# Optimization experiments

Measured on AMD Instinct MI355X. Metric: run time of the kernel, lower is better.

The kernel has to match this reference:

```python
import jax, jax.numpy as jnp
import numpy as np

D = 1024
H = 16
HD = D // H
S = 2048
B = 2
INNER = 4 * D
EPS = 1e-5


def _layernorm(x, w, b):
    mu = jnp.mean(x, axis=-1, keepdims=True)
    var = jnp.mean(jnp.square(x - mu), axis=-1, keepdims=True)
    return (x - mu) * jax.lax.rsqrt(var + EPS) * w + b


def _rope(x, cos, sin):
    # x: [B, S, H, HD]; cos/sin: [S, HD//2]
    xe, xo = x[..., 0::2], x[..., 1::2]
    c = cos[None, :, None, :]
    s = sin[None, :, None, :]
    oe = xe * c - xo * s
    oo = xe * s + xo * c
    return jnp.stack([oe, oo], axis=-1).reshape(x.shape)


def setup_inputs() -> dict:
    key = jax.random.key(0)
    ks = jax.random.split(key, 12)
    hidden_states = jax.random.normal(ks[0], (B, S, D), dtype=jnp.float32)
    time_step_emb = jax.random.normal(ks[1], (B, 6 * D), dtype=jnp.float32)
    # causal additive mask [1,1,S,S]
    causal = jnp.tril(jnp.ones((S, S), dtype=bool))
    attention_mask = jnp.where(causal, 0.0, -1e9).astype(jnp.float32)[None, None]
    # proper RoPE tables
    inv_freq = 1.0 / (10000.0 ** (np.arange(0, HD, 2, dtype=np.float32) / HD))
    t = np.arange(S, dtype=np.float32)
    freqs = np.outer(t, inv_freq)  # [S, HD//2]
    rope_cos = jnp.asarray(np.cos(freqs))
    rope_sin = jnp.asarray(np.sin(freqs))
    p = 0.02
    params = dict(
        ln1_w=jnp.ones((D,), jnp.float32), ln1_b=jnp.zeros((D,), jnp.float32),
        ln2_w=jnp.ones((D,), jnp.float32), ln2_b=jnp.zeros((D,), jnp.float32),
        c_attn_w=jax.random.normal(ks[2], (D, 3 * D), jnp.float32) * p,
        c_attn_b=jnp.zeros((3 * D,), jnp.float32),
        c_proj_w=jax.random.normal(ks[3], (D, D), jnp.float32) * p,
        c_proj_b=jnp.zeros((D,), jnp.float32),
        fc_w=jax.random.normal(ks[4], (D, INNER), jnp.float32) * p,
        fc_b=jnp.zeros((INNER,), jnp.float32),
        proj_w=jax.random.normal(ks[5], (INNER, D), jnp.float32) * p,
        proj_b=jnp.zeros((D,), jnp.float32),
        scale_shift_table=jax.random.normal(ks[6], (6, D), jnp.float32) / np.sqrt(D),
    )
    return dict(hidden_states=hidden_states, attention_mask=attention_mask,
                time_step_emb=time_step_emb, rope_cos=rope_cos, rope_sin=rope_sin,
                **params)


def reference(hidden_states, attention_mask, time_step_emb, rope_cos, rope_sin,
              ln1_w, ln1_b, ln2_w, ln2_b, c_attn_w, c_attn_b, c_proj_w, c_proj_b,
              fc_w, fc_b, proj_w, proj_b, scale_shift_table):
    b = hidden_states.shape[0]
    mods = scale_shift_table[None] + time_step_emb.reshape(b, 6, D)  # [B,6,D]
    sh_msa, sc_msa, g_msa, sh_mlp, sc_mlp, g_mlp = [mods[:, i:i + 1] for i in range(6)]

    residual = hidden_states
    h = _layernorm(hidden_states, ln1_w, ln1_b) * (1.0 + sc_msa) + sh_msa

    qkv = h @ c_attn_w + c_attn_b  # [B,S,3D]
    q, k, v = jnp.split(qkv, 3, axis=-1)
    q = _rope(q.reshape(b, S, H, HD), rope_cos, rope_sin)
    k = _rope(k.reshape(b, S, H, HD), rope_cos, rope_sin)
    v = v.reshape(b, S, H, HD)
    scores = jnp.einsum('bqhd,bkhd->bhqk', q, k) / np.sqrt(float(HD))
    scores = scores + attention_mask
    attn = jax.nn.softmax(scores, axis=-1)
    out = jnp.einsum('bhqk,bkhd->bqhd', attn, v).reshape(b, S, D)
    attn_out = out @ c_proj_w + c_proj_b

    hidden = attn_out * g_msa + residual
    residual = hidden
    h = _layernorm(hidden, ln2_w, ln2_b) * (1.0 + sc_mlp) + sh_mlp
    h = jax.nn.gelu(h @ fc_w + fc_b, approximate=True)  # gelu_new (tanh approx)
    h = h @ proj_w + proj_b
    return h * g_mlp + residual
```

## Files before the change

### kernel.cpp

```cpp
#include <hip/hip_runtime.h>
#include <hip/hip_bf16.h>
#include <type_traits>

#define D_MODEL 1024
#define N_HEADS 16
#define HEAD_DIM 64
#define SEQ 2048
#define BATCH 2
#define INNER_DIM 4096
#define ROWS (BATCH*SEQ)

using f32x4  = __attribute__((ext_vector_type(4))) float;
using bf16x8 = __attribute__((ext_vector_type(8))) short;

__device__ __forceinline__ void gl_lds16(const void* g, void* l) {
  __builtin_amdgcn_global_load_lds(
      (const __attribute__((address_space(1))) void*)g,
      (__attribute__((address_space(3))) void*)l, 16, 0, 0);
}

__device__ __forceinline__ float bf2f(unsigned short u) {
  union { unsigned int i; float f; } v; v.i = ((unsigned int)u) << 16; return v.f;
}
__device__ __forceinline__ unsigned short f2bf(float f) {
  union { float f; unsigned int i; } v; v.f = f;
  unsigned int x = v.i;
  return (unsigned short)((x + 0x7fffu + ((x >> 16) & 1u)) >> 16);
}

__device__ __forceinline__ float exp2fast(float x) {
  return __builtin_amdgcn_exp2f(x);
}

__device__ __forceinline__ float gelu_tanh(float x) {
  float x3 = x * x * x;
  float z = 0.7978845608028654f * (x + 0.044715f * x3);
  z = fminf(z, 15.0f);
  float e = __expf(2.0f * z);
  float th = (e - 1.0f) / (e + 1.0f);
  return 0.5f * x * (1.0f + th);
}

__global__ void transpose_convert(const float* __restrict__ in,
                                  unsigned short* __restrict__ out,
                                  int K, int N) {
  __shared__ float tile[32][33];
  int n0 = blockIdx.x * 32, k0 = blockIdx.y * 32;
  int tx = threadIdx.x, ty = threadIdx.y;
#pragma unroll
  for (int i = 0; i < 4; i++)
    tile[ty + i * 8][tx] = in[(size_t)(k0 + ty + i * 8) * N + n0 + tx];
  __syncthreads();
#pragma unroll
  for (int i = 0; i < 4; i++)
    out[(size_t)(n0 + ty + i * 8) * K + k0 + tx] = f2bf(tile[tx][ty + i * 8]);
}

template<int SH_IDX, int SC_IDX>
__global__ void ln_mod_kernel(const float* __restrict__ x,
                              const float* __restrict__ lw,
                              const float* __restrict__ lb,
                              const float* __restrict__ sst,
                              const float* __restrict__ temb,
                              unsigned short* __restrict__ out) {
  int row = blockIdx.x;
  int b = row >> 11;
  int t = threadIdx.x;
  const float* xr = x + (size_t)row * D_MODEL;
  float4 v = ((const float4*)xr)[t];
  float s = v.x + v.y + v.z + v.w;
  float s2 = v.x * v.x + v.y * v.y + v.z * v.z + v.w * v.w;
#pragma unroll
  for (int o = 1; o < 64; o <<= 1) { s += __shfl_xor(s, o); s2 += __shfl_xor(s2, o); }
  __shared__ float red[8];
  int wid = t >> 6, lane = t & 63;
  if (lane == 0) { red[wid] = s; red[4 + wid] = s2; }
  __syncthreads();
  s = red[0] + red[1] + red[2] + red[3];
  s2 = red[4] + red[5] + red[6] + red[7];
  float mu = s * (1.0f / D_MODEL);
  float var = s2 * (1.0f / D_MODEL) - mu * mu;
  float rs = rsqrtf(var + 1e-5f);
  int d0 = t * 4;
  float xv[4] = { v.x, v.y, v.z, v.w };
  ushort4 ov;
  unsigned short* po = (unsigned short*)&ov;
#pragma unroll
  for (int j = 0; j < 4; j++) {
    int d = d0 + j;
    float ln = (xv[j] - mu) * rs * lw[d] + lb[d];
    float sc = sst[SC_IDX * D_MODEL + d] + temb[b * 6 * D_MODEL + SC_IDX * D_MODEL + d];
    float sh = sst[SH_IDX * D_MODEL + d] + temb[b * 6 * D_MODEL + SH_IDX * D_MODEL + d];
    po[j] = f2bf(ln * (1.0f + sc) + sh);
  }
  *((ushort4*)(out + (size_t)row * D_MODEL + d0)) = ov;
}

enum { EPI_QKV = 0, EPI_GELU = 2, EPI_PART = 3 };

template<int EPI, int NK>
__global__ __launch_bounds__(512, 2)
void gemm8p(const unsigned short* __restrict__ A,
            const unsigned short* __restrict__ Bt,
            const float* __restrict__ bias,
            void* __restrict__ Cout,
            int N, int Kstride,
            const float* __restrict__ cosb,
            const float* __restrict__ sinb) {
  extern __shared__ char smem[];
  const int t = threadIdx.x;
  const int w = t >> 6, l = t & 63;
  const int lg = l >> 4, ll = l & 15;
  const int wm = w >> 2, wn = w & 3;

  const int nx = gridDim.x;
  const int nwg = nx * gridDim.y;
  const int lid = blockIdx.y * nx + blockIdx.x;
  const int nid = (lid & 7) * (nwg >> 3) + (lid >> 3);
  const int m0 = (nid / nx) * 256, n0 = (nid % nx) * 256;

  f32x4 acc[8][4] = {};

  const unsigned short* gA[2][2];
  const unsigned short* gB[2][2];
#pragma unroll
  for (int j = 0; j < 2; j++) {
    int c = j * 512 + t, row = c >> 2, ch = c & 3;
    int ks = (ch ^ ((row >> 1) & 3)) << 3;
#pragma unroll
    for (int kh = 0; kh < 2; kh++) {
      gA[kh][j] = A  + (size_t)(m0 + row) * Kstride + kh * 32 + ks;
      gB[kh][j] = Bt + (size_t)(n0 + row) * Kstride + kh * 32 + ks;
    }
  }
  unsigned aoff[8], boff[4];
#pragma unroll
  for (int mf = 0; mf < 8; mf++) {
    int row = wm * 128 + mf * 16 + ll;
    aoff[mf] = row * 64 + ((lg ^ ((row >> 1) & 3)) << 4);
  }
#pragma unroll
  for (int nf = 0; nf < 4; nf++) {
    int row = wn * 64 + nf * 16 + ll;
    boff[nf] = 65536 + row * 64 + ((lg ^ ((row >> 1) & 3)) << 4);
  }

  auto stgA = [&](int kh, int P) {
#pragma unroll
    for (int j = 0; j < 2; j++) {
      gl_lds16(gA[kh][j], smem + P * 32768 + kh * 16384 + (j * 512 + t) * 16);
      gA[kh][j] += 64;
    }
  };
  auto stgB = [&](int kh, int P) {
#pragma unroll
    for (int j = 0; j < 2; j++) {
      gl_lds16(gB[kh][j], smem + 65536 + P * 32768 + kh * 16384 + (j * 512 + t) * 16);
      gB[kh][j] += 64;
    }
  };
  auto mm = [&](int mfb, bf16x8 (&af)[4], bf16x8 (&bk)[4]) {
#pragma unroll
    for (int i = 0; i < 4; i++)
#pragma unroll
      for (int nf = 0; nf < 4; nf++)
        acc[mfb + i][nf] =
            __builtin_amdgcn_mfma_f32_16x16x32_bf16(af[i], bk[nf], acc[mfb + i][nf], 0, 0, 0);
  };

#define GBAR()  asm volatile("" ::: "memory"); __builtin_amdgcn_s_barrier(); \
                asm volatile("" ::: "memory");
#define LGKM0() asm volatile("s_waitcnt lgkmcnt(0)" ::: "memory"); \
                __builtin_amdgcn_sched_barrier(0);

  auto tile = [&](auto PC, bool stg, bool last) {
    constexpr int P = decltype(PC)::value;
    const char* ab = smem + P * 32768;
    bf16x8 af[4], bk[4];
    if (stg) stgA(0, P ^ 1);
    GBAR();
#pragma unroll
    for (int i = 0; i < 4; i++) af[i] = *(const bf16x8*)(ab + aoff[i]);
#pragma unroll
    for (int i = 0; i < 4; i++) bk[i] = *(const bf16x8*)(ab + boff[i]);
    LGKM0();
    __builtin_amdgcn_s_setprio(1); mm(0, af, bk); __builtin_amdgcn_s_setprio(0);
    GBAR();
    if (stg) stgB(0, P ^ 1);
    if (!last) asm volatile("s_waitcnt vmcnt(4)" ::: "memory");
    else       asm volatile("s_waitcnt vmcnt(0)" ::: "memory");
    GBAR();
#pragma unroll
    for (int i = 0; i < 4; i++) af[i] = *(const bf16x8*)(ab + aoff[4 + i]);
    LGKM0();
    __builtin_amdgcn_s_setprio(1); mm(4, af, bk); __builtin_amdgcn_s_setprio(0);
    GBAR();
    if (stg) stgA(1, P ^ 1);
    GBAR();
#pragma unroll
    for (int i = 0; i < 4; i++) af[i] = *(const bf16x8*)(ab + 16384 + aoff[i]);
#pragma unroll
    for (int i = 0; i < 4; i++) bk[i] = *(const bf16x8*)(ab + 16384 + boff[i]);
    LGKM0();
    __builtin_amdgcn_s_setprio(1); mm(0, af, bk); __builtin_amdgcn_s_setprio(0);
    GBAR();
    if (stg) {
      stgB(1, P ^ 1);
      asm volatile("s_waitcnt vmcnt(4)" ::: "memory");
    }
    GBAR();
#pragma unroll
    for (int i = 0; i < 4; i++) af[i] = *(const bf16x8*)(ab + 16384 + aoff[4 + i]);
    LGKM0();
    __builtin_amdgcn_s_setprio(1); mm(4, af, bk); __builtin_amdgcn_s_setprio(0);
    GBAR();
  };

  stgA(0, 0); stgB(0, 0); stgA(1, 0); stgB(1, 0);
  asm volatile("s_waitcnt vmcnt(4)" ::: "memory");
  GBAR();

#pragma unroll 1
  for (int u = 0; u + 2 < NK; u += 2) {
    tile(std::integral_constant<int, 0>{}, true, false);
    tile(std::integral_constant<int, 1>{}, true, false);
  }
  tile(std::integral_constant<int, 0>{}, true, false);
  tile(std::integral_constant<int, 1>{}, false, true);

#pragma unroll
  for (int mf = 0; mf < 8; mf++) {
#pragma unroll
    for (int nf = 0; nf < 4; nf++) {
      int col = n0 + wn * 64 + nf * 16 + ll;
      float bv = (EPI == EPI_PART) ? 0.0f : bias[col];
#pragma unroll
      for (int r = 0; r < 4; r++) {
        int row = m0 + wm * 128 + mf * 16 + lg * 4 + r;
        float v = acc[mf][nf][r] + bv;
        if constexpr (EPI == EPI_QKV) {
          if (col < 2048) {
            float vp = __shfl_xor(v, 1);
            int sp = row & (SEQ - 1);
            int ip = (col & 63) >> 1;
            float cz = cosb[sp * 32 + ip], sz = sinb[sp * 32 + ip];
            float ov = (col & 1) ? (vp * sz + v * cz) : (v * cz - vp * sz);
            if (col < 1024) ov *= 0.18033688011112042f;
            v = ov;
          }
          ((unsigned short*)Cout)[(size_t)row * N + col] = f2bf(v);
        } else if constexpr (EPI == EPI_GELU) {
          ((unsigned short*)Cout)[(size_t)row * N + col] = f2bf(gelu_tanh(v));
        } else {
          ((unsigned short*)Cout)[(size_t)row * N + col] = f2bf(v);
        }
      }
    }
  }
}
#undef GBAR
#undef LGKM0

template<int EPI, int NK>
__global__ __launch_bounds__(256, 2)
void gemm64(const unsigned short* __restrict__ A,
            const unsigned short* __restrict__ Bt,
            const float* __restrict__ bias,
            void* C0, void* C1,
            int N, int Kstride,
            const float* __restrict__ cosb,
            const float* __restrict__ sinb) {
  __shared__ unsigned short Alds[2][128 * 64];
  __shared__ unsigned short Blds[2][128 * 64];
  const int t = threadIdx.x;
  const int w = t >> 6, l = t & 63;
  const int lg = l >> 4, ll = l & 15;
  const int wm = w >> 1, wn = w & 1;
  const int kbase = blockIdx.z * (NK * 64);

  const int nx = gridDim.x;
  const int nwg = nx * gridDim.y;
  const int lid = blockIdx.y * nx + blockIdx.x;
  const int nid = (lid & 7) * (nwg >> 3) + (lid >> 3);
  const int m0 = (nid / nx) * 128, n0 = (nid % nx) * 128;

  void* Cout = blockIdx.z ? C1 : C0;

  f32x4 acc[4][4] = {};

  const unsigned short* ga[4];
  const unsigned short* gb[4];
#pragma unroll
  for (int i = 0; i < 4; i++) {
    int c = i * 256 + t, row = c >> 3, q = c & 7;
    ga[i] = A + (size_t)(m0 + row) * Kstride + kbase + ((q ^ (row & 7)) << 3);
    gb[i] = Bt + (size_t)(n0 + row) * Kstride + kbase + ((q ^ (row & 7)) << 3);
  }
  const unsigned short* ra[4][2];
  const unsigned short* rb[4][2];
#pragma unroll
  for (int f = 0; f < 4; f++) {
    int rowA = wm * 64 + f * 16 + ll;
    int rowB = wn * 64 + f * 16 + ll;
#pragma unroll
    for (int kk = 0; kk < 2; kk++) {
      ra[f][kk] = &Alds[0][rowA * 64 + ((((kk * 4 + lg) ^ (rowA & 7))) << 3)];
      rb[f][kk] = &Blds[0][rowB * 64 + ((((kk * 4 + lg) ^ (rowB & 7))) << 3)];
    }
  }

#pragma unroll
  for (int i = 0; i < 4; i++) {
    gl_lds16(ga[i], (char*)&Alds[0][0] + (i * 256 + t) * 16); ga[i] += 64;
  }
#pragma unroll
  for (int i = 0; i < 4; i++) {
    gl_lds16(gb[i], (char*)&Blds[0][0] + (i * 256 + t) * 16); gb[i] += 64;
  }

  auto giter = [&](auto BUFC, bool last) {
    constexpr int BUF = decltype(BUFC)::value;
    constexpr int NBUF = BUF ^ 1;
    if (!last) {
#pragma unroll
      for (int i = 0; i < 4; i++) {
        gl_lds16(ga[i], (char*)&Alds[NBUF][0] + (i * 256 + t) * 16); ga[i] += 64;
      }
#pragma unroll
      for (int i = 0; i < 4; i++) {
        gl_lds16(gb[i], (char*)&Blds[NBUF][0] + (i * 256 + t) * 16); gb[i] += 64;
      }
      asm volatile("s_waitcnt vmcnt(8)" ::: "memory");
    } else {
      asm volatile("s_waitcnt vmcnt(0)" ::: "memory");
    }
    __builtin_amdgcn_s_barrier();
    asm volatile("" ::: "memory");
#pragma unroll
    for (int kk = 0; kk < 2; kk++) {
      bf16x8 af[4], bfr[4];
#pragma unroll
      for (int mf = 0; mf < 4; mf++)
        af[mf] = *(const bf16x8*)(ra[mf][kk] + BUF * 8192);
#pragma unroll
      for (int nf = 0; nf < 4; nf++)
        bfr[nf] = *(const bf16x8*)(rb[nf][kk] + BUF * 8192);
#pragma unroll
      for (int mf = 0; mf < 4; mf++)
#pragma unroll
        for (int nf = 0; nf < 4; nf++)
          acc[mf][nf] = __builtin_amdgcn_mfma_f32_16x16x32_bf16(af[mf], bfr[nf], acc[mf][nf], 0, 0, 0);
    }
    asm volatile("" ::: "memory");
    __builtin_amdgcn_s_barrier();
  };

#pragma unroll 1
  for (int u = 0; u < NK - 2; u += 2) {
    giter(std::integral_constant<int, 0>{}, false);
    giter(std::integral_constant<int, 1>{}, false);
  }
  giter(std::integral_constant<int, 0>{}, false);
  giter(std::integral_constant<int, 1>{}, true);

#pragma unroll
  for (int mf = 0; mf < 4; mf++) {
#pragma unroll
    for (int nf = 0; nf < 4; nf++) {
      int col = n0 + wn * 64 + nf * 16 + ll;
#pragma unroll
      for (int r = 0; r < 4; r++) {
        int row = m0 + wm * 64 + mf * 16 + lg * 4 + r;
        float v = acc[mf][nf][r];
        ((unsigned short*)Cout)[(size_t)row * N + col] = f2bf(v);
      }
    }
  }
}

__global__ void reduce_ln(const unsigned short* __restrict__ p0,
                          const unsigned short* __restrict__ p1,
                          const float* __restrict__ bias,
                          const float* __restrict__ sst,
                          const float* __restrict__ temb,
                          const float* __restrict__ resid,
                          float* __restrict__ hidden,
                          const float* __restrict__ lw,
                          const float* __restrict__ lb,
                          unsigned short* __restrict__ hln) {
  int row = blockIdx.x, b = row >> 11, t = threadIdx.x;
  size_t base = (size_t)row * D_MODEL + t * 4;
  int col = t * 4;
  ushort4 a0 = *(const ushort4*)(p0 + base);
  ushort4 a1 = *(const ushort4*)(p1 + base);
  float4 rv = *(const float4*)(resid + base);
  const unsigned short* s0 = (const unsigned short*)&a0;
  const unsigned short* s1 = (const unsigned short*)&a1;
  const float* pr = (const float*)&rv;
  float h[4];
  float s = 0.0f, s2 = 0.0f;
#pragma unroll
  for (int j = 0; j < 4; j++) {
    int d = col + j;
    float g = sst[2 * D_MODEL + d] + temb[b * 6 * D_MODEL + 2 * D_MODEL + d];
    float v = (bf2f(s0[j]) + bf2f(s1[j]) + bias[d]) * g + pr[j];
    h[j] = v; s += v; s2 += v * v;
  }
  float4 hv; hv.x = h[0]; hv.y = h[1]; hv.z = h[2]; hv.w = h[3];
  *(float4*)(hidden + base) = hv;
#pragma unroll
  for (int o = 1; o < 64; o <<= 1) { s += __shfl_xor(s, o); s2 += __shfl_xor(s2, o); }
  __shared__ float red[8];
  int wid = t >> 6, lane = t & 63;
  if (lane == 0) { red[wid] = s; red[4 + wid] = s2; }
  __syncthreads();
  s = red[0] + red[1] + red[2] + red[3];
  s2 = red[4] + red[5] + red[6] + red[7];
  float mu = s * (1.0f / D_MODEL);
  float var = s2 * (1.0f / D_MODEL) - mu * mu;
  float rs = rsqrtf(var + 1e-5f);
  ushort4 ov;
  unsigned short* po = (unsigned short*)&ov;
#pragma unroll
  for (int j = 0; j < 4; j++) {
    int d = col + j;
    float ln = (h[j] - mu) * rs * lw[d] + lb[d];
    float sc = sst[4 * D_MODEL + d] + temb[b * 6 * D_MODEL + 4 * D_MODEL + d];
    float sh = sst[3 * D_MODEL + d] + temb[b * 6 * D_MODEL + 3 * D_MODEL + d];
    po[j] = f2bf(ln * (1.0f + sc) + sh);
  }
  *(ushort4*)(hln + base) = ov;
}

__global__ void reduce_gated(const unsigned short* __restrict__ p0,
                             const unsigned short* __restrict__ p1,
                             const float* __restrict__ bias,
                             const float* __restrict__ sst,
                             const float* __restrict__ temb,
                             int g_idx,
                             const float* __restrict__ resid,
                             float* __restrict__ out) {
  int i = blockIdx.x * 256 + threadIdx.x;
  int idx = i * 4;
  int col = idx & 1023;
  int b = idx >> 21;
  ushort4 a0 = *(const ushort4*)(p0 + idx);
  ushort4 a1 = *(const ushort4*)(p1 + idx);
  float4 rv = *(const float4*)(resid + idx);
  float4 o;
  const unsigned short* s0 = (const unsigned short*)&a0;
  const unsigned short* s1 = (const unsigned short*)&a1;
  float* po = (float*)&o;
  const float* pr = (const float*)&rv;
#pragma unroll
  for (int j = 0; j < 4; j++) {
    float s = bf2f(s0[j]) + bf2f(s1[j]) + bias[col + j];
    float g = sst[g_idx * D_MODEL + col + j] + temb[b * 6 * D_MODEL + g_idx * D_MODEL + col + j];
    po[j] = s * g + pr[j];
  }
  *(float4*)(out + idx) = o;
}

__global__ __launch_bounds__(256, 4)
void attn_kernel(const unsigned short* __restrict__ qkv,
                 unsigned short* __restrict__ attn_o) {
  __shared__ unsigned short Klds[2][64 * 64];
  __shared__ unsigned short Vt[2][64 * 64];
  __shared__ unsigned short Plds[4][16 * 64];

  const int id = blockIdx.x;
  const int bh = id & 31;
  const int b = bh >> 4, h = bh & 15;
  const int q0 = (31 - (id >> 5)) * 64;
  const int t = threadIdx.x;
  const int w = t >> 6, l = t & 63;
  const int lg = l >> 4, ll = l & 15;
  const int qw0 = q0 + w * 16;
  const int q_lane = qw0 + ll;

  bf16x8 qf[2];
  {
    const unsigned short* qb = qkv + (size_t)(b * SEQ + q_lane) * 3072 + h * 64;
    qf[0] = *(const bf16x8*)(qb + lg * 8);
    qf[1] = *(const bf16x8*)(qb + 32 + lg * 8);
  }

  const int kp = t & 31, dg = t >> 5;

  f32x4 oacc[4] = {};
  float mrun = -1e30f, lrun = 0.0f;

  {
#pragma unroll
    for (int i = 0; i < 2; i++) {
      int c = i * 256 + t;
      int kr = c >> 3, cc = c & 7;
      gl_lds16(qkv + (size_t)(b * SEQ + kr) * 3072 + 1024 + h * 64 + (cc ^ (kr & 7)) * 8,
               (char*)&Klds[0][0] + c * 16);
    }
    const unsigned short* vp = qkv + (size_t)(b * SEQ + 2 * kp) * 3072 + 2048 + h * 64 + dg * 8;
    union { uint4 u; unsigned short s[8]; } a0, a1;
    a0.u = *(const uint4*)vp;
    a1.u = *(const uint4*)(vp + 3072);
    unsigned int* vt32 = (unsigned int*)&Vt[0][0];
#pragma unroll
    for (int i = 0; i < 8; i++)
      vt32[(dg * 8 + i) * 32 + (((kp >> 2) ^ i) << 2) + (kp & 3)] =
          (unsigned int)a0.s[i] | ((unsigned int)a1.s[i] << 16);
  }
  __syncthreads();

  int buf = 0;
  for (int k0 = 0; k0 <= q0; k0 += 64) {
    const bool has_next = (k0 + 64 <= q0);
    union { uint4 u; unsigned short s[8]; } n0, n1;
    if (has_next) {
#pragma unroll
      for (int i = 0; i < 2; i++) {
        int c = i * 256 + t;
        int kr = c >> 3, cc = c & 7;
        gl_lds16(qkv + (size_t)(b * SEQ + k0 + 64 + kr) * 3072 + 1024 + h * 64 + (cc ^ (kr & 7)) * 8,
                 (char*)&Klds[buf ^ 1][0] + c * 16);
      }
      const unsigned short* vp =
          qkv + (size_t)(b * SEQ + k0 + 64 + 2 * kp) * 3072 + 2048 + h * 64 + dg * 8;
      n0.u = *(const uint4*)vp;
      n1.u = *(const uint4*)(vp + 3072);
    }

    f32x4 s[4] = {};
#pragma unroll
    for (int kk = 0; kk < 2; kk++) {
#pragma unroll
      for (int nf = 0; nf < 4; nf++) {
        int key = nf * 16 + ll;
        int cc = (kk * 4 + lg) ^ (key & 7);
        bf16x8 kf = *(const bf16x8*)((const char*)&Klds[buf][0] + key * 128 + cc * 16);
        s[nf] = __builtin_amdgcn_mfma_f32_16x16x32_bf16(kf, qf[kk], s[nf], 0, 0, 0);
      }
    }
    if (k0 == q0) {
#pragma unroll
      for (int nf = 0; nf < 4; nf++) {
        int key = k0 + nf * 16 + lg * 4;
#pragma unroll
        for (int r = 0; r < 4; r++)
          if (key + r > q_lane) s[nf][r] = -1e30f;
      }
    }
    float mx = -1e30f;
#pragma unroll
    for (int nf = 0; nf < 4; nf++)
#pragma unroll
      for (int r = 0; r < 4; r++) mx = fmaxf(mx, s[nf][r]);
    mx = fmaxf(mx, __shfl_xor(mx, 16));
    mx = fmaxf(mx, __shfl_xor(mx, 32));
    float mnew = fmaxf(mrun, mx);
    float alpha = exp2fast(mrun - mnew);
    mrun = mnew;
    float ps = 0.0f;
#pragma unroll
    for (int nf = 0; nf < 4; nf++)
#pragma unroll
      for (int r = 0; r < 4; r++) {
        float p = exp2fast(s[nf][r] - mnew);
        s[nf][r] = p;
        ps += p;
      }
    ps += __shfl_xor(ps, 16);
    ps += __shfl_xor(ps, 32);
    lrun = lrun * alpha + ps;
#pragma unroll
    for (int nf = 0; nf < 4; nf++)
#pragma unroll
      for (int r = 0; r < 4; r++) oacc[nf][r] *= alpha;

#pragma unroll
    for (int nf = 0; nf < 4; nf++) {
      unsigned int lo = (unsigned int)f2bf(s[nf][0]) | ((unsigned int)f2bf(s[nf][1]) << 16);
      unsigned int hi = (unsigned int)f2bf(s[nf][2]) | ((unsigned int)f2bf(s[nf][3]) << 16);
      int chunk = (nf * 2 + (lg >> 1)) ^ (ll & 7);
      uint2 pv; pv.x = lo; pv.y = hi;
      *(uint2*)((char*)&Plds[w][0] + ll * 128 + chunk * 16 + (lg & 1) * 8) = pv;
    }
    bf16x8 pb[2];
#pragma unroll
    for (int kk = 0; kk < 2; kk++) {
      int pc = (kk * 4 + lg) ^ (ll & 7);
      pb[kk] = *(const bf16x8*)((char*)&Plds[w][0] + ll * 128 + pc * 16);
    }
#pragma unroll
    for (int nf = 0; nf < 4; nf++) {
      int d = nf * 16 + ll;
#pragma unroll
      for (int kk = 0; kk < 2; kk++) {
        int vc = (kk * 4 + lg) ^ (d & 7);
        bf16x8 vb = *(const bf16x8*)((const char*)&Vt[buf][0] + d * 128 + vc * 16);
        oacc[nf] = __builtin_amdgcn_mfma_f32_16x16x32_bf16(vb, pb[kk], oacc[nf], 0, 0, 0);
      }
    }
    if (has_next) {
      unsigned int* vt32 = (unsigned int*)&Vt[buf ^ 1][0];
#pragma unroll
      for (int i = 0; i < 8; i++)
        vt32[(dg * 8 + i) * 32 + (((kp >> 2) ^ i) << 2) + (kp & 3)] =
            (unsigned int)n0.s[i] | ((unsigned int)n1.s[i] << 16);
    }
    __syncthreads();
    buf ^= 1;
  }

  float rl = 1.0f / lrun;
#pragma unroll
  for (int nf = 0; nf < 4; nf++) {
    ushort4 ov;
    ov.x = f2bf(oacc[nf][0] * rl);
    ov.y = f2bf(oacc[nf][1] * rl);
    ov.z = f2bf(oacc[nf][2] * rl);
    ov.w = f2bf(oacc[nf][3] * rl);
    *(ushort4*)(attn_o + (size_t)(b * SEQ + q_lane) * D_MODEL + h * 64 + nf * 16 + lg * 4) = ov;
  }
}

extern "C" void kernel_launch(void* const* d_in, const int* in_sizes, int n_in,
                              void* d_out, int out_size, void* d_ws, size_t ws_size,
                              hipStream_t stream) {
  const float* hidden_states = (const float*)d_in[0];
  const float* temb     = (const float*)d_in[2];
  const float* rope_cos = (const float*)d_in[3];
  const float* rope_sin = (const float*)d_in[4];
  const float* ln1_w    = (const float*)d_in[5];
  const float* ln1_b    = (const float*)d_in[6];
  const float* ln2_w    = (const float*)d_in[7];
  const float* ln2_b    = (const float*)d_in[8];
  const float* c_attn_w = (const float*)d_in[9];
  const float* c_attn_b = (const float*)d_in[10];
  const float* c_proj_w = (const float*)d_in[11];
  const float* c_proj_b = (const float*)d_in[12];
  const float* fc_w     = (const float*)d_in[13];
  const float* fc_b     = (const float*)d_in[14];
  const float* proj_w   = (const float*)d_in[15];
  const float* proj_b   = (const float*)d_in[16];
  const float* sst      = (const float*)d_in[17];

  char* ws = (char*)d_ws;
  unsigned short* wqkv  = (unsigned short*)(ws + 0);
  unsigned short* wproj = (unsigned short*)(ws + 6291456);
  unsigned short* wfc   = (unsigned short*)(ws + 8388608);
  unsigned short* wp2   = (unsigned short*)(ws + 16777216);
  unsigned short* hln   = (unsigned short*)(ws + 25165824);
  unsigned short* qkvb  = (unsigned short*)(ws + 33554432);
  unsigned short* attno = (unsigned short*)(ws + 58720256);
  float*          hidden = (float*)(ws + 67108864);
  unsigned short* rp0 = (unsigned short*)(ws + 33554432);
  unsigned short* rp1 = (unsigned short*)(ws + 41943040);
  unsigned short* h3  = (unsigned short*)(ws + 33554432);
  unsigned short* fp0 = (unsigned short*)(ws + 0);
  unsigned short* fp1 = (unsigned short*)(ws + 8388608);

  dim3 tb(32, 8);
  transpose_convert<<<dim3(3072 / 32, 1024 / 32), tb, 0, stream>>>(c_attn_w, wqkv, 1024, 3072);
  transpose_convert<<<dim3(1024 / 32, 1024 / 32), tb, 0, stream>>>(c_proj_w, wproj, 1024, 1024);
  transpose_convert<<<dim3(4096 / 32, 1024 / 32), tb, 0, stream>>>(fc_w, wfc, 1024, 4096);
  transpose_convert<<<dim3(1024 / 32, 4096 / 32), tb, 0, stream>>>(proj_w, wp2, 4096, 1024);

  ln_mod_kernel<0, 1><<<ROWS, 256, 0, stream>>>(hidden_states, ln1_w, ln1_b, sst, temb, hln);

  gemm8p<EPI_QKV, 16><<<dim3(3072 / 256, ROWS / 256, 1), 512, 131072, stream>>>(
      hln, wqkv, c_attn_b, qkvb, 3072, 1024, rope_cos, rope_sin);

  attn_kernel<<<dim3(32 * 32), 256, 0, stream>>>(qkvb, attno);

  gemm64<EPI_PART, 8><<<dim3(1024 / 128, ROWS / 128, 2), 256, 0, stream>>>(
      attno, wproj, c_proj_b, rp0, rp1, 1024, 1024, nullptr, nullptr);
  reduce_ln<<<ROWS, 256, 0, stream>>>(
      rp0, rp1, c_proj_b, sst, temb, hidden_states, hidden, ln2_w, ln2_b, hln);

  gemm8p<EPI_GELU, 16><<<dim3(4096 / 256, ROWS / 256, 1), 512, 131072, stream>>>(
      hln, wfc, fc_b, h3, 4096, 1024, nullptr, nullptr);

  gemm64<EPI_PART, 32><<<dim3(1024 / 128, ROWS / 128, 2), 256, 0, stream>>>(
      h3, wp2, proj_b, fp0, fp1, 1024, 4096, nullptr, nullptr);
  reduce_gated<<<(ROWS * D_MODEL / 4) / 256, 256, 0, stream>>>(
      fp0, fp1, proj_b, sst, temb, 5, hidden, (float*)d_out);
}
```

Before: 278.5 us.

## Merge weight transposes, prefetch LDS fragments earlier, switch QKV GEMM to gemm64

Merges the four weight transpose/convert launches into a single kernel that dispatches on block index, which removes launch overhead. In gemm8p, the LDS fragment reads are moved ahead of the global-to-LDS staging and barriers so they overlap with memory traffic. The QKV projection now runs on the smaller 128-tile gemm64 instead of gemm8p, with a new epilogue for bias, RoPE via lane shuffle and Q scaling, plus a GELU epilogue. The gemm64 path has lower per-block throughput but fills the machine with more blocks.

```diff
diff --git a/kernel.cpp b/kernel.cpp
--- a/kernel.cpp
+++ b/kernel.cpp
@@ -41,11 +41,18 @@
   return 0.5f * x * (1.0f + th);
 }
 
-__global__ void transpose_convert(const float* __restrict__ in,
-                                  unsigned short* __restrict__ out,
-                                  int K, int N) {
+__global__ void transpose_all(const float* __restrict__ w0, const float* __restrict__ w1,
+                              const float* __restrict__ w2, const float* __restrict__ w3,
+                              unsigned short* __restrict__ o0, unsigned short* __restrict__ o1,
+                              unsigned short* __restrict__ o2, unsigned short* __restrict__ o3) {
   __shared__ float tile[32][33];
-  int n0 = blockIdx.x * 32, k0 = blockIdx.y * 32;
+  int bid = blockIdx.x;
+  const float* in; unsigned short* out; int K, N, nx;
+  if (bid < 3072)      { in = w0; out = o0; K = 1024; N = 3072; nx = 96; }
+  else if (bid < 4096) { in = w1; out = o1; K = 1024; N = 1024; nx = 32; bid -= 3072; }
+  else if (bid < 8192) { in = w2; out = o2; K = 1024; N = 4096; nx = 128; bid -= 4096; }
+  else                 { in = w3; out = o3; K = 4096; N = 1024; nx = 32; bid -= 8192; }
+  int n0 = (bid % nx) * 32, k0 = (bid / nx) * 32;
   int tx = threadIdx.x, ty = threadIdx.y;
 #pragma unroll
   for (int i = 0; i < 4; i++)
@@ -98,6 +105,11 @@
 
 enum { EPI_QKV = 0, EPI_GELU = 2, EPI_PART = 3 };
 
+#define GBAR()  asm volatile("" ::: "memory"); __builtin_amdgcn_s_barrier(); \
+                asm volatile("" ::: "memory");
+#define LGKM0() asm volatile("s_waitcnt lgkmcnt(0)" ::: "memory"); \
+                __builtin_amdgcn_sched_barrier(0);
+
 template<int EPI, int NK>
 __global__ __launch_bounds__(512, 2)
 void gemm8p(const unsigned short* __restrict__ A,
@@ -168,49 +180,44 @@
             __builtin_amdgcn_mfma_f32_16x16x32_bf16(af[i], bk[nf], acc[mfb + i][nf], 0, 0, 0);
   };
 
-#define GBAR()  asm volatile("" ::: "memory"); __builtin_amdgcn_s_barrier(); \
-                asm volatile("" ::: "memory");
-#define LGKM0() asm volatile("s_waitcnt lgkmcnt(0)" ::: "memory"); \
-                __builtin_amdgcn_sched_barrier(0);
-
   auto tile = [&](auto PC, bool stg, bool last) {
     constexpr int P = decltype(PC)::value;
     const char* ab = smem + P * 32768;
     bf16x8 af[4], bk[4];
+#pragma unroll
+    for (int i = 0; i < 4; i++) af[i] = *(const bf16x8*)(ab + aoff[i]);
+#pragma unroll
+    for (int i = 0; i < 4; i++) bk[i] = *(const bf16x8*)(ab + boff[i]);
     if (stg) stgA(0, P ^ 1);
     GBAR();
-#pragma unroll
-    for (int i = 0; i < 4; i++) af[i] = *(const bf16x8*)(ab + aoff[i]);
-#pragma unroll
-    for (int i = 0; i < 4; i++) bk[i] = *(const bf16x8*)(ab + boff[i]);
     LGKM0();
     __builtin_amdgcn_s_setprio(1); mm(0, af, bk); __builtin_amdgcn_s_setprio(0);
     GBAR();
+#pragma unroll
+    for (int i = 0; i < 4; i++) af[i] = *(const bf16x8*)(ab + aoff[4 + i]);
     if (stg) stgB(0, P ^ 1);
     if (!last) asm volatile("s_waitcnt vmcnt(4)" ::: "memory");
     else       asm volatile("s_waitcnt vmcnt(0)" ::: "memory");
     GBAR();
-#pragma unroll
-    for (int i = 0; i < 4; i++) af[i] = *(const bf16x8*)(ab + aoff[4 + i]);
     LGKM0();
     __builtin_amdgcn_s_setprio(1); mm(4, af, bk); __builtin_amdgcn_s_setprio(0);
     GBAR();
+#pragma unroll
+    for (int i = 0; i < 4; i++) af[i] = *(const bf16x8*)(ab + 16384 + aoff[i]);
+#pragma unroll
+    for (int i = 0; i < 4; i++) bk[i] = *(const bf16x8*)(ab + 16384 + boff[i]);
     if (stg) stgA(1, P ^ 1);
     GBAR();
-#pragma unroll
-    for (int i = 0; i < 4; i++) af[i] = *(const bf16x8*)(ab + 16384 + aoff[i]);
-#pragma unroll
-    for (int i = 0; i < 4; i++) bk[i] = *(const bf16x8*)(ab + 16384 + boff[i]);
     LGKM0();
     __builtin_amdgcn_s_setprio(1); mm(0, af, bk); __builtin_amdgcn_s_setprio(0);
     GBAR();
+#pragma unroll
+    for (int i = 0; i < 4; i++) af[i] = *(const bf16x8*)(ab + 16384 + aoff[4 + i]);
     if (stg) {
       stgB(1, P ^ 1);
       asm volatile("s_waitcnt vmcnt(4)" ::: "memory");
     }
     GBAR();
-#pragma unroll
-    for (int i = 0; i < 4; i++) af[i] = *(const bf16x8*)(ab + 16384 + aoff[4 + i]);
     LGKM0();
     __builtin_amdgcn_s_setprio(1); mm(4, af, bk); __builtin_amdgcn_s_setprio(0);
     GBAR();
@@ -368,11 +375,27 @@
 #pragma unroll
     for (int nf = 0; nf < 4; nf++) {
       int col = n0 + wn * 64 + nf * 16 + ll;
+      float bv = (EPI == EPI_PART) ? 0.0f : bias[col];
 #pragma unroll
       for (int r = 0; r < 4; r++) {
         int row = m0 + wm * 64 + mf * 16 + lg * 4 + r;
-        float v = acc[mf][nf][r];
-        ((unsigned short*)Cout)[(size_t)row * N + col] = f2bf(v);
+        float v = acc[mf][nf][r] + bv;
+        if constexpr (EPI == EPI_QKV) {
+          if (col < 2048) {
+            float vp = __shfl_xor(v, 1);
+            int sp = row & (SEQ - 1);
+            int ip = (col & 63) >> 1;
+            float cz = cosb[sp * 32 + ip], sz = sinb[sp * 32 + ip];
+            float ov = (col & 1) ? (vp * sz + v * cz) : (v * cz - vp * sz);
+            if (col < 1024) ov *= 0.18033688011112042f;
+            v = ov;
+          }
+          ((unsigned short*)Cout)[(size_t)row * N + col] = f2bf(v);
+        } else if constexpr (EPI == EPI_GELU) {
+          ((unsigned short*)Cout)[(size_t)row * N + col] = f2bf(gelu_tanh(v));
+        } else {
+          ((unsigned short*)Cout)[(size_t)row * N + col] = f2bf(v);
+        }
       }
     }
   }
@@ -659,15 +682,13 @@
   unsigned short* fp1 = (unsigned short*)(ws + 8388608);
 
   dim3 tb(32, 8);
-  transpose_convert<<<dim3(3072 / 32, 1024 / 32), tb, 0, stream>>>(c_attn_w, wqkv, 1024, 3072);
-  transpose_convert<<<dim3(1024 / 32, 1024 / 32), tb, 0, stream>>>(c_proj_w, wproj, 1024, 1024);
-  transpose_convert<<<dim3(4096 / 32, 1024 / 32), tb, 0, stream>>>(fc_w, wfc, 1024, 4096);
-  transpose_convert<<<dim3(1024 / 32, 4096 / 32), tb, 0, stream>>>(proj_w, wp2, 4096, 1024);
+  transpose_all<<<12288, tb, 0, stream>>>(c_attn_w, c_proj_w, fc_w, proj_w,
+                                          wqkv, wproj, wfc, wp2);
 
   ln_mod_kernel<0, 1><<<ROWS, 256, 0, stream>>>(hidden_states, ln1_w, ln1_b, sst, temb, hln);
 
-  gemm8p<EPI_QKV, 16><<<dim3(3072 / 256, ROWS / 256, 1), 512, 131072, stream>>>(
-      hln, wqkv, c_attn_b, qkvb, 3072, 1024, rope_cos, rope_sin);
+  gemm64<EPI_QKV, 16><<<dim3(3072 / 128, ROWS / 128, 1), 256, 0, stream>>>(
+      hln, wqkv, c_attn_b, qkvb, qkvb, 3072, 1024, rope_cos, rope_sin);
 
   attn_kernel<<<dim3(32 * 32), 256, 0, stream>>>(qkvb, attno);
 
```

Result: faster. 244.4 us (-12.2%).
